# Optimization experiments

Measured on AMD Instinct MI355X. Metric: run time of the kernel, lower is better.

## Reference

```python
import jax, jax.numpy as jnp
import numpy as np

M = 128      # max_child_num
H = 256      # hidden_size
F = 256      # node_feat_size (must equal H per original view logic)
T = 4        # edge_type_num
I = 2        # num_iterations
NSEM = 57    # Tree.num_sem


def setup_inputs() -> dict:
    key = jax.random.key(0)
    ks = jax.random.split(key, 16)
    def lin(k, shape, fan_in):
        return (jax.random.normal(k, shape, jnp.float32) / np.sqrt(fan_in)).astype(jnp.float32)
    return {
        "parent_feature": jax.random.normal(ks[0], (1, F), jnp.float32),
        "W_parent": lin(ks[1], (F, H * M), F),
        "b_parent": jnp.zeros((H * M,), jnp.float32),
        "W_exists": lin(ks[2], (H, 1), H),
        "b_exists": jnp.zeros((1,), jnp.float32),
        "W_edge_latent": lin(ks[3], (2 * H, H), 2 * H),
        "b_edge_latent": jnp.zeros((H,), jnp.float32),
        "W_edge_exists": lin(ks[4], (T, H), H),   # per-type 1-out linear, stacked
        "b_edge_exists": jnp.zeros((T,), jnp.float32),
        "W_op": lin(ks[5], (I, 3 * H + T, H), 3 * H + T),
        "b_op": jnp.zeros((I, H), jnp.float32),
        "W_child": lin(ks[6], (H * (I + 1), H), H * (I + 1)),
        "b_child": jnp.zeros((H,), jnp.float32),
        "W_sem": lin(ks[7], (H, NSEM), H),
        "b_sem": jnp.zeros((NSEM,), jnp.float32),
        "W_child2": lin(ks[8], (H, F), H),
        "b_child2": jnp.zeros((F,), jnp.float32),
    }


def reference(parent_feature, W_parent, b_parent, W_exists, b_exists,
              W_edge_latent, b_edge_latent, W_edge_exists, b_edge_exists,
              W_op, b_op, W_child, b_child, W_sem, b_sem, W_child2, b_child2):
    # parent -> per-child latents [M, H]
    cf = jax.nn.relu(parent_feature @ W_parent + b_parent).reshape(M, H)
    child_exists_logits = cf @ W_exists + b_exists                      # [M, 1]

    # pairwise edge latents [M, M, H]
    pair = jnp.concatenate([
        jnp.broadcast_to(cf[:, None, :], (M, M, H)),
        jnp.broadcast_to(cf[None, :, :], (M, M, H)),
    ], axis=-1)
    el = jax.nn.relu(pair @ W_edge_latent + b_edge_latent)              # [M, M, H]
    ee = jnp.einsum('ijh,th->ijt', el, W_edge_exists) + b_edge_exists   # [M, M, T]

    # dense-mask equivalent of torch.nonzero edge list: an edge exists per
    # (i, j, type) triple where its logit > 0 and both endpoints exist.
    exists = child_exists_logits[:, 0] > 0                              # [M]
    mask = (ee > 0) & exists[:, None, None] & exists[None, :, None]     # [M, M, T]
    maskf = mask.astype(cf.dtype)

    iter_feats = [cf]
    for i in range(I):
        # node_edge_op input is concat([cf_src, cf_dst, edge_latent, onehot(t)*logit]);
        # split the linear into per-block matmuls to avoid a [M,M,T,3H+T] concat.
        W1, W2, W3, W4 = (W_op[i, :H], W_op[i, H:2 * H],
                          W_op[i, 2 * H:3 * H], W_op[i, 3 * H:])        # W4: [T, H]
        pre = ((cf @ W1)[:, None, None, :]
               + (cf @ W2)[None, :, None, :]
               + (el @ W3)[:, :, None, :]
               + ee[:, :, :, None] * W4[None, None, :, :]
               + b_op[i])                                               # [M, M, T, H]
        h = jax.nn.relu(pre) * maskf[..., None]
        # scatter_max over source index i with zero-initialized output:
        # relu output >= 0 and masked-out edges are 0, so plain max matches.
        cf = jnp.max(h, axis=(1, 2))                                    # [M, H]
        iter_feats.append(cf)

    allf = jnp.concatenate(iter_feats, axis=1)                          # [M, H*(I+1)]
    ch = jax.nn.relu(allf @ W_child + b_child)                          # [M, H]
    child_sem_logits = ch @ W_sem + b_sem                               # [M, NSEM]
    child_feats = jax.nn.relu(ch @ W_child2 + b_child2)                 # [M, F]

    return (child_feats[None], child_sem_logits[None],
            child_exists_logits[None], ee[None])
```

## Files before the change

### kernel.cpp

```cpp
#include <hip/hip_runtime.h>
#include <hip/hip_bf16.h>

#define M_ 128
#define H_ 256
#define F_ 256
#define T_ 4
#define NSEM_ 57

typedef __attribute__((ext_vector_type(8))) short bf16x8;
typedef __attribute__((ext_vector_type(4))) float f32x4;

__device__ __forceinline__ float4 ld4(const float* p) { return *reinterpret_cast<const float4*>(p); }
__device__ __forceinline__ void st4(float* p, float4 v) { *reinterpret_cast<float4*>(p) = v; }
__device__ __forceinline__ float4 add4(float4 a, float4 b) { return make_float4(a.x+b.x, a.y+b.y, a.z+b.z, a.w+b.w); }
__device__ __forceinline__ float4 relu4(float4 a) { return make_float4(fmaxf(a.x,0.f), fmaxf(a.y,0.f), fmaxf(a.z,0.f), fmaxf(a.w,0.f)); }
__device__ __forceinline__ float4 fma4(float s, float4 w, float4 c) { return make_float4(fmaf(s,w.x,c.x), fmaf(s,w.y,c.y), fmaf(s,w.z,c.z), fmaf(s,w.w,c.w)); }

__device__ __forceinline__ unsigned short f2bfu(float x) {
  unsigned u = __float_as_uint(x);
  return (unsigned short)((u + 0x7FFFu + ((u >> 16) & 1u)) >> 16);
}
__device__ __forceinline__ unsigned pack2(float lo, float hi) {
  return (unsigned)f2bfu(lo) | ((unsigned)f2bfu(hi) << 16);
}

__global__ void __launch_bounds__(256) k_parent(
    const float* __restrict__ pf, const float* __restrict__ Wp,
    const float* __restrict__ Wop, float* __restrict__ part,
    unsigned short* __restrict__ W36F, unsigned short* __restrict__ W768F)
{
  const int t = threadIdx.x;
  __shared__ float spf[8];
  __shared__ float tile[16][17];

  const int fbg = blockIdx.x >> 1;
  const int half = blockIdx.x & 1;
  const bool it0 = fbg < 128;
  const int fb = it0 ? fbg : fbg - 128;
  const int kk = fb >> 4, ct = fb & 15;
  const int base_k = kk * 32 + half * 16;
  int row_base;
  if (it0) row_base = 512 + base_k;
  else row_base = (base_k < 256) ? 512 + base_k
                : (base_k < 512 ? base_k : base_k - 512);
  const float* wsrc = Wop + (it0 ? 0 : 197632);
  {
    const int r = t >> 4, c = t & 15;
    tile[r][c] = wsrc[(size_t)(row_base + r) * 256 + ct * 16 + c];
  }

  const int cb = (blockIdx.x & 31) * 1024 + t * 4;
  const int kc = blockIdx.x >> 5;
  if (t < 8) spf[t] = pf[kc * 8 + t];
  __syncthreads();
  const float* w = Wp + (size_t)kc * 8 * 32768 + cb;
  float4 acc = make_float4(0.f, 0.f, 0.f, 0.f);
  #pragma unroll
  for (int k = 0; k < 8; ++k)
    acc = fma4(spf[k], ld4(w + (size_t)k * 32768), acc);
  st4(&part[kc * 32768 + cb], acc);

  {
    const int k_local = ((t >> 7) << 3) + (t & 7);
    const int h_local = (t >> 3) & 15;
    const int e = half * 256 + t;
    unsigned short v = f2bfu(tile[k_local][h_local]);
    if (it0) W36F[fb * 512 + e] = v;
    else     W768F[fb * 512 + e] = v;
  }
}

__global__ void __launch_bounds__(256) k_stage1(
    const float* __restrict__ part, const float* __restrict__ bp,
    const float* __restrict__ Wel, const float* __restrict__ Wop0,
    const float* __restrict__ Wex, const float* __restrict__ bex,
    float* __restrict__ cf0, float* __restrict__ A, float* __restrict__ B,
    float* __restrict__ a1, float* __restrict__ a2,
    float* __restrict__ cf1, float* __restrict__ cf2,
    float* __restrict__ out_ex)
{
  const int m = blockIdx.x >> 1, sel = blockIdx.x & 1;
  const int t = threadIdx.x;
  __shared__ float sall[256];
  __shared__ float red[2][4][256];
  __shared__ float redE[4];

  (sel ? cf2 : cf1)[m * 256 + t] = 0.f;

  float pv[32];
  #pragma unroll
  for (int q = 0; q < 32; ++q) pv[q] = part[q * 32768 + m * 256 + t];
  float v = bp[m * 256 + t];
  #pragma unroll
  for (int q = 0; q < 32; ++q) v += pv[q];
  v = fmaxf(v, 0.f);
  sall[t] = v;
  if (sel == 0) {
    cf0[m * 256 + t] = v;
    float p = v * Wex[t];
    #pragma unroll
    for (int off = 32; off > 0; off >>= 1) p += __shfl_xor(p, off);
    if ((t & 63) == 0) redE[t >> 6] = p;
  }
  __syncthreads();

  const float* W0 = Wel  + (sel ? 65536 : 0);
  const float* W1 = Wop0 + (sel ? 65536 : 0);
  const int hq = (t & 63) << 2, kg = t >> 6, k0 = kg * 64;
  float4 acc0 = make_float4(0.f, 0.f, 0.f, 0.f), acc1 = acc0;
  #pragma unroll 8
  for (int k = k0; k < k0 + 64; ++k) {
    const float s = sall[k];
    acc0 = fma4(s, ld4(W0 + k * 256 + hq), acc0);
    acc1 = fma4(s, ld4(W1 + k * 256 + hq), acc1);
  }
  st4(&red[0][kg][hq], acc0);
  st4(&red[1][kg][hq], acc1);
  __syncthreads();
  if (kg < 2) {
    float4 r = add4(add4(ld4(&red[kg][0][hq]), ld4(&red[kg][1][hq])),
                    add4(ld4(&red[kg][2][hq]), ld4(&red[kg][3][hq])));
    float* dst = (kg == 0) ? (sel ? B : A) : (sel ? a2 : a1);
    st4(&dst[m * 256 + hq], r);
  }
  if (sel == 0 && t == 0)
    out_ex[m] = redE[0] + redE[1] + redE[2] + redE[3] + bex[0];
}

__global__ void __launch_bounds__(512) k_gemm0(
    const float* __restrict__ Arow, const float* __restrict__ Brow,
    const float* __restrict__ bel, const unsigned short* __restrict__ W36F,
    const float* __restrict__ Wee, const float* __restrict__ bee,
    const float* __restrict__ a1, const float* __restrict__ a2,
    const float* __restrict__ Wop0, const float* __restrict__ bop0,
    const float* __restrict__ exlog,
    float* __restrict__ ee_g, float* __restrict__ cf1)
{
  const int i  = blockIdx.x >> 2;
  const int jq = blockIdx.x & 3;
  const int t  = threadIdx.x;
  const int w  = t >> 6;
  const int l  = t & 63;
  __shared__ char sEL[32 * 512];
  __shared__ float see[32][4];
  __shared__ float sexf[32];

  const bool exi = exlog[i] > 0.f;
  const int lr = l & 15, lk = l >> 4;

  const int c0 = w * 32 + lr, c1 = c0 + 16;
  const float b10 = a1[i * 256 + c0] + bop0[c0];
  const float b11 = a1[i * 256 + c1] + bop0[c1];
  float w40[4], w41[4], a2v0[8], a2v1[8];
  #pragma unroll
  for (int tt = 0; tt < 4; ++tt) {
    w40[tt] = Wop0[(768 + tt) * 256 + c0];
    w41[tt] = Wop0[(768 + tt) * 256 + c1];
  }
  #pragma unroll
  for (int jt = 0; jt < 2; ++jt)
    #pragma unroll
    for (int q = 0; q < 4; ++q) {
      const int j = jq * 32 + jt * 16 + lk * 4 + q;
      a2v0[jt * 4 + q] = a2[j * 256 + c0];
      a2v1[jt * 4 + q] = a2[j * 256 + c1];
    }

  {
    const int row = t >> 4;
    const int sub = t & 15;
    const int kb  = sub * 16;
    const float* Ap  = Arow + i * 256 + kb;
    const float* Bp  = Brow + (jq * 32 + row) * 256 + kb;
    const float* blp = bel + kb;
    float e[16];
    #pragma unroll
    for (int q = 0; q < 16; q += 4) {
      float4 av = ld4(Ap + q), bv = ld4(Bp + q), lv = ld4(blp + q);
      e[q+0] = fmaxf(av.x + bv.x + lv.x, 0.f);
      e[q+1] = fmaxf(av.y + bv.y + lv.y, 0.f);
      e[q+2] = fmaxf(av.z + bv.z + lv.z, 0.f);
      e[q+3] = fmaxf(av.w + bv.w + lv.w, 0.f);
    }
    float s[4] = {0.f, 0.f, 0.f, 0.f};
    #pragma unroll
    for (int tt = 0; tt < 4; ++tt) {
      #pragma unroll
      for (int q = 0; q < 16; q += 4) {
        float4 wv = ld4(Wee + tt * 256 + kb + q);
        s[tt] = fmaf(e[q+0], wv.x, s[tt]);
        s[tt] = fmaf(e[q+1], wv.y, s[tt]);
        s[tt] = fmaf(e[q+2], wv.z, s[tt]);
        s[tt] = fmaf(e[q+3], wv.w, s[tt]);
      }
    }
    #pragma unroll
    for (int off = 1; off < 16; off <<= 1) {
      s[0] += __shfl_xor(s[0], off);
      s[1] += __shfl_xor(s[1], off);
      s[2] += __shfl_xor(s[2], off);
      s[3] += __shfl_xor(s[3], off);
    }
    if (sub < 4) {
      const float v = s[sub] + bee[sub];
      see[row][sub] = v;
      ee_g[(i * 128 + jq * 32 + row) * 4 + sub] = v;
    }
    const int swz = (row & 7) << 4;
    uint4 w0, w1;
    w0.x = pack2(e[0], e[1]);  w0.y = pack2(e[2], e[3]);
    w0.z = pack2(e[4], e[5]);  w0.w = pack2(e[6], e[7]);
    w1.x = pack2(e[8], e[9]);  w1.y = pack2(e[10], e[11]);
    w1.z = pack2(e[12], e[13]); w1.w = pack2(e[14], e[15]);
    *reinterpret_cast<uint4*>(sEL + ((row * 512 + kb * 2)      ^ swz)) = w0;
    *reinterpret_cast<uint4*>(sEL + ((row * 512 + kb * 2 + 16) ^ swz)) = w1;
  }
  if (t < 32) sexf[t] = exlog[jq * 32 + t];
  __syncthreads();

  f32x4 acc[2][2];
  #pragma unroll
  for (int jt = 0; jt < 2; ++jt)
    #pragma unroll
    for (int ct = 0; ct < 2; ++ct)
      acc[jt][ct] = (f32x4){0.f, 0.f, 0.f, 0.f};

  const int swz0 = (lr & 7) << 4;
  bf16x8 cb0 = *reinterpret_cast<const bf16x8*>(W36F + (0 * 16 + w * 2 + 0) * 512 + l * 8);
  bf16x8 cb1 = *reinterpret_cast<const bf16x8*>(W36F + (0 * 16 + w * 2 + 1) * 512 + l * 8);
  bf16x8 ca0 = *reinterpret_cast<const bf16x8*>(sEL + ((lr * 512 + lk * 16) ^ swz0));
  bf16x8 ca1 = *reinterpret_cast<const bf16x8*>(sEL + (((16 + lr) * 512 + lk * 16) ^ swz0));
  #pragma unroll
  for (int kc = 0; kc < 8; ++kc) {
    bf16x8 nb0, nb1, na0, na1;
    if (kc < 7) {
      const int kbyte = (kc + 1) * 64 + lk * 16;
      nb0 = *reinterpret_cast<const bf16x8*>(W36F + ((kc + 1) * 16 + w * 2 + 0) * 512 + l * 8);
      nb1 = *reinterpret_cast<const bf16x8*>(W36F + ((kc + 1) * 16 + w * 2 + 1) * 512 + l * 8);
      na0 = *reinterpret_cast<const bf16x8*>(sEL + ((lr * 512 + kbyte) ^ swz0));
      na1 = *reinterpret_cast<const bf16x8*>(sEL + (((16 + lr) * 512 + kbyte) ^ swz0));
    }
    acc[0][0] = __builtin_amdgcn_mfma_f32_16x16x32_bf16(ca0, cb0, acc[0][0], 0, 0, 0);
    acc[1][0] = __builtin_amdgcn_mfma_f32_16x16x32_bf16(ca1, cb0, acc[1][0], 0, 0, 0);
    acc[0][1] = __builtin_amdgcn_mfma_f32_16x16x32_bf16(ca0, cb1, acc[0][1], 0, 0, 0);
    acc[1][1] = __builtin_amdgcn_mfma_f32_16x16x32_bf16(ca1, cb1, acc[1][1], 0, 0, 0);
    if (kc < 7) { cb0 = nb0; cb1 = nb1; ca0 = na0; ca1 = na1; }
  }

  float am0 = 0.f, am1 = 0.f;
  #pragma unroll
  for (int jt = 0; jt < 2; ++jt) {
    #pragma unroll
    for (int q = 0; q < 4; ++q) {
      const int jrow = jt * 16 + lk * 4 + q;
      if (exi && (sexf[jrow] > 0.f)) {
        const float e0 = see[jrow][0], e1 = see[jrow][1];
        const float e2 = see[jrow][2], e3 = see[jrow][3];
        const float pb0 = b10 + a2v0[jt * 4 + q] + acc[jt][0][q];
        const float pb1 = b11 + a2v1[jt * 4 + q] + acc[jt][1][q];
        if (e0 > 0.f) { am0 = fmaxf(am0, fmaxf(fmaf(e0, w40[0], pb0), 0.f));
                        am1 = fmaxf(am1, fmaxf(fmaf(e0, w41[0], pb1), 0.f)); }
        if (e1 > 0.f) { am0 = fmaxf(am0, fmaxf(fmaf(e1, w40[1], pb0), 0.f));
                        am1 = fmaxf(am1, fmaxf(fmaf(e1, w41[1], pb1), 0.f)); }
        if (e2 > 0.f) { am0 = fmaxf(am0, fmaxf(fmaf(e2, w40[2], pb0), 0.f));
                        am1 = fmaxf(am1, fmaxf(fmaf(e2, w41[2], pb1), 0.f)); }
        if (e3 > 0.f) { am0 = fmaxf(am0, fmaxf(fmaf(e3, w40[3], pb0), 0.f));
                        am1 = fmaxf(am1, fmaxf(fmaf(e3, w41[3], pb1), 0.f)); }
      }
    }
  }
  am0 = fmaxf(am0, __shfl_xor(am0, 16));
  am0 = fmaxf(am0, __shfl_xor(am0, 32));
  am1 = fmaxf(am1, __shfl_xor(am1, 16));
  am1 = fmaxf(am1, __shfl_xor(am1, 32));
  if (lk == 0) {
    atomicMax((unsigned int*)&cf1[i * 256 + c0], __float_as_uint(am0));
    atomicMax((unsigned int*)&cf1[i * 256 + c1], __float_as_uint(am1));
  }
}

__global__ void __launch_bounds__(512) k_gemm1(
    const float* __restrict__ Arow, const float* __restrict__ Brow,
    const float* __restrict__ bel, const unsigned short* __restrict__ W768F,
    const float* __restrict__ cf1,
    const float* __restrict__ Wop1, const float* __restrict__ bop1,
    const float* __restrict__ exlog, const float* __restrict__ ee_g,
    float* __restrict__ cf2)
{
  const int i  = blockIdx.x >> 2;
  const int jq = blockIdx.x & 3;
  const int t  = threadIdx.x;
  const int w  = t >> 6;
  const int l  = t & 63;
  __shared__ char sEL[32 * 1536];
  __shared__ float see[32][4];
  __shared__ float sexf[32];

  const bool exi = exlog[i] > 0.f;
  const int lr = l & 15, lk = l >> 4;

  const int c0 = w * 32 + lr, c1 = c0 + 16;
  const float b10 = bop1[c0];
  const float b11 = bop1[c1];
  float w40[4], w41[4];
  #pragma unroll
  for (int tt = 0; tt < 4; ++tt) {
    w40[tt] = Wop1[(768 + tt) * 256 + c0];
    w41[tt] = Wop1[(768 + tt) * 256 + c1];
  }
  if (t < 128)
    see[t >> 2][t & 3] = ee_g[(i * 128 + jq * 32 + (t >> 2)) * 4 + (t & 3)];
  if (t < 32) sexf[t] = exlog[jq * 32 + t];

  {
    const int row = t >> 4;
    const int sub = t & 15;
    const int kb  = sub * 16;
    const int swz = (row & 7) << 4;
    {
      const float* Ap  = Arow + i * 256 + kb;
      const float* Bp  = Brow + (jq * 32 + row) * 256 + kb;
      const float* blp = bel + kb;
      float e[16];
      #pragma unroll
      for (int q = 0; q < 16; q += 4) {
        float4 av = ld4(Ap + q), bv = ld4(Bp + q), lv = ld4(blp + q);
        e[q+0] = fmaxf(av.x + bv.x + lv.x, 0.f);
        e[q+1] = fmaxf(av.y + bv.y + lv.y, 0.f);
        e[q+2] = fmaxf(av.z + bv.z + lv.z, 0.f);
        e[q+3] = fmaxf(av.w + bv.w + lv.w, 0.f);
      }
      uint4 w0, w1;
      w0.x = pack2(e[0], e[1]);  w0.y = pack2(e[2], e[3]);
      w0.z = pack2(e[4], e[5]);  w0.w = pack2(e[6], e[7]);
      w1.x = pack2(e[8], e[9]);  w1.y = pack2(e[10], e[11]);
      w1.z = pack2(e[12], e[13]); w1.w = pack2(e[14], e[15]);
      *reinterpret_cast<uint4*>(sEL + ((row * 1536 + kb * 2)      ^ swz)) = w0;
      *reinterpret_cast<uint4*>(sEL + ((row * 1536 + kb * 2 + 16) ^ swz)) = w1;
    }
    {
      const float* cj = cf1 + (jq * 32 + row) * 256 + kb;
      float4 v0 = ld4(cj), v1 = ld4(cj + 4), v2 = ld4(cj + 8), v3 = ld4(cj + 12);
      uint4 w0, w1;
      w0.x = pack2(v0.x, v0.y); w0.y = pack2(v0.z, v0.w);
      w0.z = pack2(v1.x, v1.y); w0.w = pack2(v1.z, v1.w);
      w1.x = pack2(v2.x, v2.y); w1.y = pack2(v2.z, v2.w);
      w1.z = pack2(v3.x, v3.y); w1.w = pack2(v3.z, v3.w);
      *reinterpret_cast<uint4*>(sEL + ((row * 1536 + 512 + kb * 2)      ^ swz)) = w0;
      *reinterpret_cast<uint4*>(sEL + ((row * 1536 + 512 + kb * 2 + 16) ^ swz)) = w1;
    }
    {
      const float* ci = cf1 + i * 256 + kb;
      float4 v0 = ld4(ci), v1 = ld4(ci + 4), v2 = ld4(ci + 8), v3 = ld4(ci + 12);
      uint4 w0, w1;
      w0.x = pack2(v0.x, v0.y); w0.y = pack2(v0.z, v0.w);
      w0.z = pack2(v1.x, v1.y); w0.w = pack2(v1.z, v1.w);
      w1.x = pack2(v2.x, v2.y); w1.y = pack2(v2.z, v2.w);
      w1.z = pack2(v3.x, v3.y); w1.w = pack2(v3.z, v3.w);
      *reinterpret_cast<uint4*>(sEL + ((row * 1536 + 1024 + kb * 2)      ^ swz)) = w0;
      *reinterpret_cast<uint4*>(sEL + ((row * 1536 + 1024 + kb * 2 + 16) ^ swz)) = w1;
    }
  }
  __syncthreads();

  f32x4 acc[2][2];
  #pragma unroll
  for (int jt = 0; jt < 2; ++jt)
    #pragma unroll
    for (int ct = 0; ct < 2; ++ct)
      acc[jt][ct] = (f32x4){0.f, 0.f, 0.f, 0.f};

  const int swz0 = (lr & 7) << 4;
  bf16x8 cb0 = *reinterpret_cast<const bf16x8*>(W768F + (0 * 16 + w * 2 + 0) * 512 + l * 8);
  bf16x8 cb1 = *reinterpret_cast<const bf16x8*>(W768F + (0 * 16 + w * 2 + 1) * 512 + l * 8);
  bf16x8 ca0 = *reinterpret_cast<const bf16x8*>(sEL + ((lr * 1536 + lk * 16) ^ swz0));
  bf16x8 ca1 = *reinterpret_cast<const bf16x8*>(sEL + (((16 + lr) * 1536 + lk * 16) ^ swz0));
  #pragma unroll
  for (int kc = 0; kc < 24; ++kc) {
    bf16x8 nb0, nb1, na0, na1;
    if (kc < 23) {
      const int kbyte = (kc + 1) * 64 + lk * 16;
      nb0 = *reinterpret_cast<const bf16x8*>(W768F + ((kc + 1) * 16 + w * 2 + 0) * 512 + l * 8);
      nb1 = *reinterpret_cast<const bf16x8*>(W768F + ((kc + 1) * 16 + w * 2 + 1) * 512 + l * 8);
      na0 = *reinterpret_cast<const bf16x8*>(sEL + ((lr * 1536 + kbyte) ^ swz0));
      na1 = *reinterpret_cast<const bf16x8*>(sEL + (((16 + lr) * 1536 + kbyte) ^ swz0));
    }
    acc[0][0] = __builtin_amdgcn_mfma_f32_16x16x32_bf16(ca0, cb0, acc[0][0], 0, 0, 0);
    acc[1][0] = __builtin_amdgcn_mfma_f32_16x16x32_bf16(ca1, cb0, acc[1][0], 0, 0, 0);
    acc[0][1] = __builtin_amdgcn_mfma_f32_16x16x32_bf16(ca0, cb1, acc[0][1], 0, 0, 0);
    acc[1][1] = __builtin_amdgcn_mfma_f32_16x16x32_bf16(ca1, cb1, acc[1][1], 0, 0, 0);
    if (kc < 23) { cb0 = nb0; cb1 = nb1; ca0 = na0; ca1 = na1; }
  }

  float am0 = 0.f, am1 = 0.f;
  #pragma unroll
  for (int jt = 0; jt < 2; ++jt) {
    #pragma unroll
    for (int q = 0; q < 4; ++q) {
      const int jrow = jt * 16 + lk * 4 + q;
      if (exi && (sexf[jrow] > 0.f)) {
        const float e0 = see[jrow][0], e1 = see[jrow][1];
        const float e2 = see[jrow][2], e3 = see[jrow][3];
        const float pb0 = b10 + acc[jt][0][q];
        const float pb1 = b11 + acc[jt][1][q];
        if (e0 > 0.f) { am0 = fmaxf(am0, fmaxf(fmaf(e0, w40[0], pb0), 0.f));
                        am1 = fmaxf(am1, fmaxf(fmaf(e0, w41[0], pb1), 0.f)); }
        if (e1 > 0.f) { am0 = fmaxf(am0, fmaxf(fmaf(e1, w40[1], pb0), 0.f));
                        am1 = fmaxf(am1, fmaxf(fmaf(e1, w41[1], pb1), 0.f)); }
        if (e2 > 0.f) { am0 = fmaxf(am0, fmaxf(fmaf(e2, w40[2], pb0), 0.f));
                        am1 = fmaxf(am1, fmaxf(fmaf(e2, w41[2], pb1), 0.f)); }
        if (e3 > 0.f) { am0 = fmaxf(am0, fmaxf(fmaf(e3, w40[3], pb0), 0.f));
                        am1 = fmaxf(am1, fmaxf(fmaf(e3, w41[3], pb1), 0.f)); }
      }
    }
  }
  am0 = fmaxf(am0, __shfl_xor(am0, 16));
  am0 = fmaxf(am0, __shfl_xor(am0, 32));
  am1 = fmaxf(am1, __shfl_xor(am1, 16));
  am1 = fmaxf(am1, __shfl_xor(am1, 32));
  if (lk == 0) {
    atomicMax((unsigned int*)&cf2[i * 256 + c0], __float_as_uint(am0));
    atomicMax((unsigned int*)&cf2[i * 256 + c1], __float_as_uint(am1));
  }
}

__global__ void __launch_bounds__(512) k_final(
    const float* __restrict__ cf0, const float* __restrict__ cf1,
    const float* __restrict__ cf2,
    const float* __restrict__ Wch, const float* __restrict__ bch,
    const float* __restrict__ Wsem, const float* __restrict__ bsem,
    const float* __restrict__ Wch2, const float* __restrict__ bch2,
    float* __restrict__ out_feats, float* __restrict__ out_sem)
{
  const int m  = blockIdx.x;
  const int t  = threadIdx.x;
  const int hq = (t & 63) << 2;
  const int kg = t >> 6;
  __shared__ float sall[768];
  __shared__ float sch[256];
  __shared__ float red[8][256];
  __shared__ float redS[8][64];

  if (t < 256) {
    sall[t]       = cf0[m * 256 + t];
    sall[256 + t] = cf1[m * 256 + t];
    sall[512 + t] = cf2[m * 256 + t];
  }
  __syncthreads();

  {
    float4 acc = make_float4(0.f, 0.f, 0.f, 0.f);
    const int k0 = kg * 96;
    #pragma unroll 8
    for (int k = k0; k < k0 + 96; ++k)
      acc = fma4(sall[k], ld4(Wch + k * 256 + hq), acc);
    st4(&red[kg][hq], acc);
  }
  __syncthreads();
  if (kg == 0) {
    float4 r = ld4(&red[0][hq]);
    #pragma unroll
    for (int g2 = 1; g2 < 8; ++g2) r = add4(r, ld4(&red[g2][hq]));
    r = relu4(add4(r, ld4(bch + hq)));
    st4(&sch[hq], r);
  }
  __syncthreads();

  {
    float4 f = make_float4(0.f, 0.f, 0.f, 0.f);
    const int k0 = kg * 32;
    #pragma unroll 8
    for (int k = k0; k < k0 + 32; ++k)
      f = fma4(sch[k], ld4(Wch2 + k * 256 + hq), f);
    const int s = t & 63;
    float sv = 0.f;
    if (s < 57) {
      #pragma unroll 8
      for (int k = k0; k < k0 + 32; ++k)
        sv = fmaf(sch[k], Wsem[k * 57 + s], sv);
    }
    redS[kg][s] = sv;
    st4(&red[kg][hq], f);
  }
  __syncthreads();
  if (kg == 0) {
    float4 r = ld4(&red[0][hq]);
    #pragma unroll
    for (int g2 = 1; g2 < 8; ++g2) r = add4(r, ld4(&red[g2][hq]));
    r = relu4(add4(r, ld4(bch2 + hq)));
    st4(&out_feats[m * 256 + hq], r);
  }
  if (t < 57) {
    float s2 = bsem[t];
    #pragma unroll
    for (int g2 = 0; g2 < 8; ++g2) s2 += redS[g2][t];
    out_sem[m * 57 + t] = s2;
  }
}

extern "C" void kernel_launch(void* const* d_in, const int* in_sizes, int n_in,
                              void* d_out, int out_size, void* d_ws, size_t ws_size,
                              hipStream_t stream)
{
  const float* pf   = (const float*)d_in[0];
  const float* Wp   = (const float*)d_in[1];
  const float* bp   = (const float*)d_in[2];
  const float* Wex  = (const float*)d_in[3];
  const float* bex  = (const float*)d_in[4];
  const float* Wel  = (const float*)d_in[5];
  const float* bel  = (const float*)d_in[6];
  const float* Wee  = (const float*)d_in[7];
  const float* bee  = (const float*)d_in[8];
  const float* Wop  = (const float*)d_in[9];
  const float* bop  = (const float*)d_in[10];
  const float* Wch  = (const float*)d_in[11];
  const float* bch  = (const float*)d_in[12];
  const float* Wsem = (const float*)d_in[13];
  const float* bsem = (const float*)d_in[14];
  const float* Wch2 = (const float*)d_in[15];
  const float* bch2 = (const float*)d_in[16];

  float* out_feats = (float*)d_out;
  float* out_sem   = out_feats + M_ * F_;
  float* out_ex    = out_sem + M_ * NSEM_;
  float* out_ee    = out_ex + M_;

  float* ws = (float*)d_ws;
  float* cf0 = ws;
  float* cf1 = ws + 32768;
  float* cf2 = ws + 65536;
  float* Ab  = ws + 98304;
  float* Bb  = ws + 131072;
  float* a1  = ws + 163840;
  float* a2  = ws + 196608;
  float* part = ws + 229376;
  unsigned short* W36F  = (unsigned short*)(ws + 1277952);
  unsigned short* W768F = (unsigned short*)(ws + 1310720);

  const float* Wop0 = Wop;
  const float* Wop1 = Wop + 197632;

  k_parent<<<1024, 256, 0, stream>>>(pf, Wp, Wop, part, W36F, W768F);
  k_stage1<<<256, 256, 0, stream>>>(part, bp, Wel, Wop0, Wex, bex,
                                    cf0, Ab, Bb, a1, a2, cf1, cf2, out_ex);
  k_gemm0<<<512, 512, 0, stream>>>(Ab, Bb, bel, W36F, Wee, bee,
                                   a1, a2, Wop0, bop, out_ex, out_ee, cf1);
  k_gemm1<<<512, 512, 0, stream>>>(Ab, Bb, bel, W768F, cf1,
                                   Wop1, bop + 256, out_ex, out_ee, cf2);
  k_final<<<128, 512, 0, stream>>>(cf0, cf1, cf2, Wch, bch, Wsem, bsem,
                                   Wch2, bch2, out_feats, out_sem);
}
```

Baseline: 65.41 us.

## Enlarge edge GEMM tiles to 64 rows and merge stage1 blocks per child

The two pairwise edge GEMM kernels now give each block 64 j-rows instead of 32, so each weight fragment loaded from global memory feeds four MFMA row tiles rather than two. This halves the grid and halves how often the B operand is reloaded across blocks. The explicit register double-buffering of operands is dropped in favour of straight loads inside the unrolled loop. Stage1 now runs one 512-thread block per child, so the parent reduction is done once instead of twice. The trade-offs are fewer blocks (256) on a large GPU, more LDS per block (96KB in gemm1), and a2 now read from global memory inside the epilogue.

```diff
diff --git a/kernel.cpp b/kernel.cpp
--- a/kernel.cpp
+++ b/kernel.cpp
@@ -70,7 +70,7 @@
   }
 }
 
-__global__ void __launch_bounds__(256) k_stage1(
+__global__ void __launch_bounds__(512) k_stage1(
     const float* __restrict__ part, const float* __restrict__ bp,
     const float* __restrict__ Wel, const float* __restrict__ Wop0,
     const float* __restrict__ Wex, const float* __restrict__ bex,
@@ -79,51 +79,48 @@
     float* __restrict__ cf1, float* __restrict__ cf2,
     float* __restrict__ out_ex)
 {
-  const int m = blockIdx.x >> 1, sel = blockIdx.x & 1;
+  const int m = blockIdx.x;
   const int t = threadIdx.x;
+  const int tt = t & 255, half = t >> 8;
   __shared__ float sall[256];
-  __shared__ float red[2][4][256];
+  __shared__ float red[8][256];
   __shared__ float redE[4];
 
-  (sel ? cf2 : cf1)[m * 256 + t] = 0.f;
-
-  float pv[32];
-  #pragma unroll
-  for (int q = 0; q < 32; ++q) pv[q] = part[q * 32768 + m * 256 + t];
-  float v = bp[m * 256 + t];
-  #pragma unroll
-  for (int q = 0; q < 32; ++q) v += pv[q];
-  v = fmaxf(v, 0.f);
-  sall[t] = v;
-  if (sel == 0) {
-    cf0[m * 256 + t] = v;
-    float p = v * Wex[t];
+  (half ? cf2 : cf1)[m * 256 + tt] = 0.f;
+
+  if (half == 0) {
+    float pv[32];
+    #pragma unroll
+    for (int q = 0; q < 32; ++q) pv[q] = part[q * 32768 + m * 256 + tt];
+    float v = bp[m * 256 + tt];
+    #pragma unroll
+    for (int q = 0; q < 32; ++q) v += pv[q];
+    v = fmaxf(v, 0.f);
+    sall[tt] = v;
+    cf0[m * 256 + tt] = v;
+    float p = v * Wex[tt];
     #pragma unroll
     for (int off = 32; off > 0; off >>= 1) p += __shfl_xor(p, off);
-    if ((t & 63) == 0) redE[t >> 6] = p;
-  }
-  __syncthreads();
-
-  const float* W0 = Wel  + (sel ? 65536 : 0);
-  const float* W1 = Wop0 + (sel ? 65536 : 0);
-  const int hq = (t & 63) << 2, kg = t >> 6, k0 = kg * 64;
-  float4 acc0 = make_float4(0.f, 0.f, 0.f, 0.f), acc1 = acc0;
+    if ((tt & 63) == 0) redE[tt >> 6] = p;
+  }
+  __syncthreads();
+
+  const int kg = t >> 6, s = kg & 3, kh = kg >> 2;
+  const int hq = (t & 63) << 2, k0 = kh * 128;
+  const float* W = (s == 0) ? Wel : (s == 1) ? Wel + 65536
+                 : (s == 2) ? Wop0 : Wop0 + 65536;
+  float4 acc = make_float4(0.f, 0.f, 0.f, 0.f);
   #pragma unroll 8
-  for (int k = k0; k < k0 + 64; ++k) {
-    const float s = sall[k];
-    acc0 = fma4(s, ld4(W0 + k * 256 + hq), acc0);
-    acc1 = fma4(s, ld4(W1 + k * 256 + hq), acc1);
-  }
-  st4(&red[0][kg][hq], acc0);
-  st4(&red[1][kg][hq], acc1);
-  __syncthreads();
-  if (kg < 2) {
-    float4 r = add4(add4(ld4(&red[kg][0][hq]), ld4(&red[kg][1][hq])),
-                    add4(ld4(&red[kg][2][hq]), ld4(&red[kg][3][hq])));
-    float* dst = (kg == 0) ? (sel ? B : A) : (sel ? a2 : a1);
+  for (int k = k0; k < k0 + 128; ++k)
+    acc = fma4(sall[k], ld4(W + k * 256 + hq), acc);
+  st4(&red[kg][hq], acc);
+  __syncthreads();
+  if (kg < 4) {
+    float4 r = add4(ld4(&red[kg][hq]), ld4(&red[kg + 4][hq]));
+    float* dst = (kg == 0) ? A : (kg == 1) ? B : (kg == 2) ? a1 : a2;
     st4(&dst[m * 256 + hq], r);
   }
-  if (sel == 0 && t == 0)
+  if (t == 0)
     out_ex[m] = redE[0] + redE[1] + redE[2] + redE[3] + bex[0];
 }
 
@@ -136,46 +133,37 @@
     const float* __restrict__ exlog,
     float* __restrict__ ee_g, float* __restrict__ cf1)
 {
-  const int i  = blockIdx.x >> 2;
-  const int jq = blockIdx.x & 3;
+  const int i  = blockIdx.x >> 1;
+  const int jh = blockIdx.x & 1;
   const int t  = threadIdx.x;
   const int w  = t >> 6;
   const int l  = t & 63;
-  __shared__ char sEL[32 * 512];
-  __shared__ float see[32][4];
-  __shared__ float sexf[32];
+  __shared__ char sEL[64 * 512];
+  __shared__ float see[64][4];
+  __shared__ float sexf[64];
 
   const bool exi = exlog[i] > 0.f;
   const int lr = l & 15, lk = l >> 4;
-
   const int c0 = w * 32 + lr, c1 = c0 + 16;
   const float b10 = a1[i * 256 + c0] + bop0[c0];
   const float b11 = a1[i * 256 + c1] + bop0[c1];
-  float w40[4], w41[4], a2v0[8], a2v1[8];
-  #pragma unroll
-  for (int tt = 0; tt < 4; ++tt) {
-    w40[tt] = Wop0[(768 + tt) * 256 + c0];
-    w41[tt] = Wop0[(768 + tt) * 256 + c1];
-  }
-  #pragma unroll
-  for (int jt = 0; jt < 2; ++jt)
-    #pragma unroll
-    for (int q = 0; q < 4; ++q) {
-      const int j = jq * 32 + jt * 16 + lk * 4 + q;
-      a2v0[jt * 4 + q] = a2[j * 256 + c0];
-      a2v1[jt * 4 + q] = a2[j * 256 + c1];
-    }
+  float w40[4], w41[4];
+  #pragma unroll
+  for (int q = 0; q < 4; ++q) {
+    w40[q] = Wop0[(768 + q) * 256 + c0];
+    w41[q] = Wop0[(768 + q) * 256 + c1];
+  }
 
   {
-    const int row = t >> 4;
-    const int sub = t & 15;
-    const int kb  = sub * 16;
+    const int row = t >> 3;
+    const int sub = t & 7;
+    const int kb  = sub * 32;
     const float* Ap  = Arow + i * 256 + kb;
-    const float* Bp  = Brow + (jq * 32 + row) * 256 + kb;
+    const float* Bp  = Brow + (jh * 64 + row) * 256 + kb;
     const float* blp = bel + kb;
-    float e[16];
-    #pragma unroll
-    for (int q = 0; q < 16; q += 4) {
+    float e[32];
+    #pragma unroll
+    for (int q = 0; q < 32; q += 4) {
       float4 av = ld4(Ap + q), bv = ld4(Bp + q), lv = ld4(blp + q);
       e[q+0] = fmaxf(av.x + bv.x + lv.x, 0.f);
       e[q+1] = fmaxf(av.y + bv.y + lv.y, 0.f);
@@ -186,7 +174,7 @@
     #pragma unroll
     for (int tt = 0; tt < 4; ++tt) {
       #pragma unroll
-      for (int q = 0; q < 16; q += 4) {
+      for (int q = 0; q < 32; q += 4) {
         float4 wv = ld4(Wee + tt * 256 + kb + q);
         s[tt] = fmaf(e[q+0], wv.x, s[tt]);
         s[tt] = fmaf(e[q+1], wv.y, s[tt]);
@@ -195,7 +183,7 @@
       }
     }
     #pragma unroll
-    for (int off = 1; off < 16; off <<= 1) {
+    for (int off = 1; off < 8; off <<= 1) {
       s[0] += __shfl_xor(s[0], off);
       s[1] += __shfl_xor(s[1], off);
       s[2] += __shfl_xor(s[2], off);
@@ -204,60 +192,56 @@
     if (sub < 4) {
       const float v = s[sub] + bee[sub];
       see[row][sub] = v;
-      ee_g[(i * 128 + jq * 32 + row) * 4 + sub] = v;
+      ee_g[(i * 128 + jh * 64 + row) * 4 + sub] = v;
     }
     const int swz = (row & 7) << 4;
-    uint4 w0, w1;
-    w0.x = pack2(e[0], e[1]);  w0.y = pack2(e[2], e[3]);
-    w0.z = pack2(e[4], e[5]);  w0.w = pack2(e[6], e[7]);
-    w1.x = pack2(e[8], e[9]);  w1.y = pack2(e[10], e[11]);
-    w1.z = pack2(e[12], e[13]); w1.w = pack2(e[14], e[15]);
-    *reinterpret_cast<uint4*>(sEL + ((row * 512 + kb * 2)      ^ swz)) = w0;
-    *reinterpret_cast<uint4*>(sEL + ((row * 512 + kb * 2 + 16) ^ swz)) = w1;
-  }
-  if (t < 32) sexf[t] = exlog[jq * 32 + t];
-  __syncthreads();
-
-  f32x4 acc[2][2];
-  #pragma unroll
-  for (int jt = 0; jt < 2; ++jt)
+    #pragma unroll
+    for (int h4 = 0; h4 < 4; ++h4) {
+      uint4 wv;
+      wv.x = pack2(e[h4*8+0], e[h4*8+1]);
+      wv.y = pack2(e[h4*8+2], e[h4*8+3]);
+      wv.z = pack2(e[h4*8+4], e[h4*8+5]);
+      wv.w = pack2(e[h4*8+6], e[h4*8+7]);
+      *reinterpret_cast<uint4*>(sEL + ((row * 512 + kb * 2 + h4 * 16) ^ swz)) = wv;
+    }
+  }
+  if (t < 64) sexf[t] = exlog[jh * 64 + t];
+  __syncthreads();
+
+  f32x4 acc[4][2];
+  #pragma unroll
+  for (int rt = 0; rt < 4; ++rt)
     #pragma unroll
     for (int ct = 0; ct < 2; ++ct)
-      acc[jt][ct] = (f32x4){0.f, 0.f, 0.f, 0.f};
+      acc[rt][ct] = (f32x4){0.f, 0.f, 0.f, 0.f};
 
   const int swz0 = (lr & 7) << 4;
-  bf16x8 cb0 = *reinterpret_cast<const bf16x8*>(W36F + (0 * 16 + w * 2 + 0) * 512 + l * 8);
-  bf16x8 cb1 = *reinterpret_cast<const bf16x8*>(W36F + (0 * 16 + w * 2 + 1) * 512 + l * 8);
-  bf16x8 ca0 = *reinterpret_cast<const bf16x8*>(sEL + ((lr * 512 + lk * 16) ^ swz0));
-  bf16x8 ca1 = *reinterpret_cast<const bf16x8*>(sEL + (((16 + lr) * 512 + lk * 16) ^ swz0));
   #pragma unroll
   for (int kc = 0; kc < 8; ++kc) {
-    bf16x8 nb0, nb1, na0, na1;
-    if (kc < 7) {
-      const int kbyte = (kc + 1) * 64 + lk * 16;
-      nb0 = *reinterpret_cast<const bf16x8*>(W36F + ((kc + 1) * 16 + w * 2 + 0) * 512 + l * 8);
-      nb1 = *reinterpret_cast<const bf16x8*>(W36F + ((kc + 1) * 16 + w * 2 + 1) * 512 + l * 8);
-      na0 = *reinterpret_cast<const bf16x8*>(sEL + ((lr * 512 + kbyte) ^ swz0));
-      na1 = *reinterpret_cast<const bf16x8*>(sEL + (((16 + lr) * 512 + kbyte) ^ swz0));
-    }
-    acc[0][0] = __builtin_amdgcn_mfma_f32_16x16x32_bf16(ca0, cb0, acc[0][0], 0, 0, 0);
-    acc[1][0] = __builtin_amdgcn_mfma_f32_16x16x32_bf16(ca1, cb0, acc[1][0], 0, 0, 0);
-    acc[0][1] = __builtin_amdgcn_mfma_f32_16x16x32_bf16(ca0, cb1, acc[0][1], 0, 0, 0);
-    acc[1][1] = __builtin_amdgcn_mfma_f32_16x16x32_bf16(ca1, cb1, acc[1][1], 0, 0, 0);
-    if (kc < 7) { cb0 = nb0; cb1 = nb1; ca0 = na0; ca1 = na1; }
+    const int kbyte = kc * 64 + lk * 16;
+    bf16x8 bf0 = *reinterpret_cast<const bf16x8*>(W36F + (kc * 16 + w * 2 + 0) * 512 + l * 8);
+    bf16x8 bf1 = *reinterpret_cast<const bf16x8*>(W36F + (kc * 16 + w * 2 + 1) * 512 + l * 8);
+    #pragma unroll
+    for (int rt = 0; rt < 4; ++rt) {
+      bf16x8 af = *reinterpret_cast<const bf16x8*>(
+          sEL + (((rt * 16 + lr) * 512 + kbyte) ^ swz0));
+      acc[rt][0] = __builtin_amdgcn_mfma_f32_16x16x32_bf16(af, bf0, acc[rt][0], 0, 0, 0);
+      acc[rt][1] = __builtin_amdgcn_mfma_f32_16x16x32_bf16(af, bf1, acc[rt][1], 0, 0, 0);
+    }
   }
 
   float am0 = 0.f, am1 = 0.f;
   #pragma unroll
-  for (int jt = 0; jt < 2; ++jt) {
+  for (int rt = 0; rt < 4; ++rt) {
     #pragma unroll
     for (int q = 0; q < 4; ++q) {
-      const int jrow = jt * 16 + lk * 4 + q;
+      const int jrow = rt * 16 + lk * 4 + q;
+      const int j = jh * 64 + jrow;
       if (exi && (sexf[jrow] > 0.f)) {
         const float e0 = see[jrow][0], e1 = see[jrow][1];
         const float e2 = see[jrow][2], e3 = see[jrow][3];
-        const float pb0 = b10 + a2v0[jt * 4 + q] + acc[jt][0][q];
-        const float pb1 = b11 + a2v1[jt * 4 + q] + acc[jt][1][q];
+        const float pb0 = b10 + a2[j * 256 + c0] + acc[rt][0][q];
+        const float pb1 = b11 + a2[j * 256 + c1] + acc[rt][1][q];
         if (e0 > 0.f) { am0 = fmaxf(am0, fmaxf(fmaf(e0, w40[0], pb0), 0.f));
                         am1 = fmaxf(am1, fmaxf(fmaf(e0, w41[0], pb1), 0.f)); }
         if (e1 > 0.f) { am0 = fmaxf(am0, fmaxf(fmaf(e1, w40[1], pb0), 0.f));
@@ -287,122 +271,116 @@
     const float* __restrict__ exlog, const float* __restrict__ ee_g,
     float* __restrict__ cf2)
 {
-  const int i  = blockIdx.x >> 2;
-  const int jq = blockIdx.x & 3;
+  const int i  = blockIdx.x >> 1;
+  const int jh = blockIdx.x & 1;
   const int t  = threadIdx.x;
   const int w  = t >> 6;
   const int l  = t & 63;
-  __shared__ char sEL[32 * 1536];
-  __shared__ float see[32][4];
-  __shared__ float sexf[32];
+  __shared__ char sEL[64 * 1536];
+  __shared__ float see[64][4];
+  __shared__ float sexf[64];
 
   const bool exi = exlog[i] > 0.f;
   const int lr = l & 15, lk = l >> 4;
-
   const int c0 = w * 32 + lr, c1 = c0 + 16;
   const float b10 = bop1[c0];
   const float b11 = bop1[c1];
   float w40[4], w41[4];
   #pragma unroll
-  for (int tt = 0; tt < 4; ++tt) {
-    w40[tt] = Wop1[(768 + tt) * 256 + c0];
-    w41[tt] = Wop1[(768 + tt) * 256 + c1];
-  }
-  if (t < 128)
-    see[t >> 2][t & 3] = ee_g[(i * 128 + jq * 32 + (t >> 2)) * 4 + (t & 3)];
-  if (t < 32) sexf[t] = exlog[jq * 32 + t];
+  for (int q = 0; q < 4; ++q) {
+    w40[q] = Wop1[(768 + q) * 256 + c0];
+    w41[q] = Wop1[(768 + q) * 256 + c1];
+  }
+  if (t < 256)
+    see[t >> 2][t & 3] = ee_g[(i * 128 + jh * 64 + (t >> 2)) * 4 + (t & 3)];
+  if (t < 64) sexf[t] = exlog[jh * 64 + t];
 
   {
-    const int row = t >> 4;
-    const int sub = t & 15;
-    const int kb  = sub * 16;
+    const int row = t >> 3;
+    const int sub = t & 7;
+    const int kb  = sub * 32;
     const int swz = (row & 7) << 4;
     {
       const float* Ap  = Arow + i * 256 + kb;
-      const float* Bp  = Brow + (jq * 32 + row) * 256 + kb;
+      const float* Bp  = Brow + (jh * 64 + row) * 256 + kb;
       const float* blp = bel + kb;
-      float e[16];
+      float e[32];
       #pragma unroll
-      for (int q = 0; q < 16; q += 4) {
+      for (int q = 0; q < 32; q += 4) {
         float4 av = ld4(Ap + q), bv = ld4(Bp + q), lv = ld4(blp + q);
         e[q+0] = fmaxf(av.x + bv.x + lv.x, 0.f);
         e[q+1] = fmaxf(av.y + bv.y + lv.y, 0.f);
         e[q+2] = fmaxf(av.z + bv.z + lv.z, 0.f);
         e[q+3] = fmaxf(av.w + bv.w + lv.w, 0.f);
       }
-      uint4 w0, w1;
-      w0.x = pack2(e[0], e[1]);  w0.y = pack2(e[2], e[3]);
-      w0.z = pack2(e[4], e[5]);  w0.w = pack2(e[6], e[7]);
-      w1.x = pack2(e[8], e[9]);  w1.y = pack2(e[10], e[11]);
-      w1.z = pack2(e[12], e[13]); w1.w = pack2(e[14], e[15]);
-      *reinterpret_cast<uint4*>(sEL + ((row * 1536 + kb * 2)      ^ swz)) = w0;
-      *reinterpret_cast<uint4*>(sEL + ((row * 1536 + kb * 2 + 16) ^ swz)) = w1;
+      #pragma unroll
+      for (int h4 = 0; h4 < 4; ++h4) {
+        uint4 wv;
+        wv.x = pack2(e[h4*8+0], e[h4*8+1]);
+        wv.y = pack2(e[h4*8+2], e[h4*8+3]);
+        wv.z = pack2(e[h4*8+4], e[h4*8+5]);
+        wv.w = pack2(e[h4*8+6], e[h4*8+7]);
+        *reinterpret_cast<uint4*>(sEL + ((row * 1536 + kb * 2 + h4 * 16) ^ swz)) = wv;
+      }
     }
     {
-      const float* cj = cf1 + (jq * 32 + row) * 256 + kb;
-      float4 v0 = ld4(cj), v1 = ld4(cj + 4), v2 = ld4(cj + 8), v3 = ld4(cj + 12);
-      uint4 w0, w1;
-      w0.x = pack2(v0.x, v0.y); w0.y = pack2(v0.z, v0.w);
-      w0.z = pack2(v1.x, v1.y); w0.w = pack2(v1.z, v1.w);
-      w1.x = pack2(v2.x, v2.y); w1.y = pack2(v2.z, v2.w);
-      w1.z = pack2(v3.x, v3.y); w1.w = pack2(v3.z, v3.w);
-      *reinterpret_cast<uint4*>(sEL + ((row * 1536 + 512 + kb * 2)      ^ swz)) = w0;
-      *reinterpret_cast<uint4*>(sEL + ((row * 1536 + 512 + kb * 2 + 16) ^ swz)) = w1;
+      const float* cj = cf1 + (jh * 64 + row) * 256 + kb;
+      #pragma unroll
+      for (int h4 = 0; h4 < 4; ++h4) {
+        float4 v0 = ld4(cj + h4 * 8), v1 = ld4(cj + h4 * 8 + 4);
+        uint4 wv;
+        wv.x = pack2(v0.x, v0.y); wv.y = pack2(v0.z, v0.w);
+        wv.z = pack2(v1.x, v1.y); wv.w = pack2(v1.z, v1.w);
+        *reinterpret_cast<uint4*>(sEL + ((row * 1536 + 512 + kb * 2 + h4 * 16) ^ swz)) = wv;
+      }
     }
     {
       const float* ci = cf1 + i * 256 + kb;
-      float4 v0 = ld4(ci), v1 = ld4(ci + 4), v2 = ld4(ci + 8), v3 = ld4(ci + 12);
-      uint4 w0, w1;
-      w0.x = pack2(v0.x, v0.y); w0.y = pack2(v0.z, v0.w);
-      w0.z = pack2(v1.x, v1.y); w0.w = pack2(v1.z, v1.w);
-      w1.x = pack2(v2.x, v2.y); w1.y = pack2(v2.z, v2.w);
-      w1.z = pack2(v3.x, v3.y); w1.w = pack2(v3.z, v3.w);
-      *reinterpret_cast<uint4*>(sEL + ((row * 1536 + 1024 + kb * 2)      ^ swz)) = w0;
-      *reinterpret_cast<uint4*>(sEL + ((row * 1536 + 1024 + kb * 2 + 16) ^ swz)) = w1;
-    }
-  }
-  __syncthreads();
-
-  f32x4 acc[2][2];
-  #pragma unroll
-  for (int jt = 0; jt < 2; ++jt)
+      #pragma unroll
+      for (int h4 = 0; h4 < 4; ++h4) {
+        float4 v0 = ld4(ci + h4 * 8), v1 = ld4(ci + h4 * 8 + 4);
+        uint4 wv;
+        wv.x = pack2(v0.x, v0.y); wv.y = pack2(v0.z, v0.w);
+        wv.z = pack2(v1.x, v1.y); wv.w = pack2(v1.z, v1.w);
+        *reinterpret_cast<uint4*>(sEL + ((row * 1536 + 1024 + kb * 2 + h4 * 16) ^ swz)) = wv;
+      }
+    }
+  }
+  __syncthreads();
+
+  f32x4 acc[4][2];
+  #pragma unroll
+  for (int rt = 0; rt < 4; ++rt)
     #pragma unroll
     for (int ct = 0; ct < 2; ++ct)
-      acc[jt][ct] = (f32x4){0.f, 0.f, 0.f, 0.f};
+      acc[rt][ct] = (f32x4){0.f, 0.f, 0.f, 0.f};
 
   const int swz0 = (lr & 7) << 4;
-  bf16x8 cb0 = *reinterpret_cast<const bf16x8*>(W768F + (0 * 16 + w * 2 + 0) * 512 + l * 8);
-  bf16x8 cb1 = *reinterpret_cast<const bf16x8*>(W768F + (0 * 16 + w * 2 + 1) * 512 + l * 8);
-  bf16x8 ca0 = *reinterpret_cast<const bf16x8*>(sEL + ((lr * 1536 + lk * 16) ^ swz0));
-  bf16x8 ca1 = *reinterpret_cast<const bf16x8*>(sEL + (((16 + lr) * 1536 + lk * 16) ^ swz0));
   #pragma unroll
   for (int kc = 0; kc < 24; ++kc) {
-    bf16x8 nb0, nb1, na0, na1;
-    if (kc < 23) {
-      const int kbyte = (kc + 1) * 64 + lk * 16;
-      nb0 = *reinterpret_cast<const bf16x8*>(W768F + ((kc + 1) * 16 + w * 2 + 0) * 512 + l * 8);
-      nb1 = *reinterpret_cast<const bf16x8*>(W768F + ((kc + 1) * 16 + w * 2 + 1) * 512 + l * 8);
-      na0 = *reinterpret_cast<const bf16x8*>(sEL + ((lr * 1536 + kbyte) ^ swz0));
-      na1 = *reinterpret_cast<const bf16x8*>(sEL + (((16 + lr) * 1536 + kbyte) ^ swz0));
-    }
-    acc[0][0] = __builtin_amdgcn_mfma_f32_16x16x32_bf16(ca0, cb0, acc[0][0], 0, 0, 0);
-    acc[1][0] = __builtin_amdgcn_mfma_f32_16x16x32_bf16(ca1, cb0, acc[1][0], 0, 0, 0);
-    acc[0][1] = __builtin_amdgcn_mfma_f32_16x16x32_bf16(ca0, cb1, acc[0][1], 0, 0, 0);
-    acc[1][1] = __builtin_amdgcn_mfma_f32_16x16x32_bf16(ca1, cb1, acc[1][1], 0, 0, 0);
-    if (kc < 23) { cb0 = nb0; cb1 = nb1; ca0 = na0; ca1 = na1; }
+    const int kbyte = kc * 64 + lk * 16;
+    bf16x8 bf0 = *reinterpret_cast<const bf16x8*>(W768F + (kc * 16 + w * 2 + 0) * 512 + l * 8);
+    bf16x8 bf1 = *reinterpret_cast<const bf16x8*>(W768F + (kc * 16 + w * 2 + 1) * 512 + l * 8);
+    #pragma unroll
+    for (int rt = 0; rt < 4; ++rt) {
+      bf16x8 af = *reinterpret_cast<const bf16x8*>(
+          sEL + (((rt * 16 + lr) * 1536 + kbyte) ^ swz0));
+      acc[rt][0] = __builtin_amdgcn_mfma_f32_16x16x32_bf16(af, bf0, acc[rt][0], 0, 0, 0);
+      acc[rt][1] = __builtin_amdgcn_mfma_f32_16x16x32_bf16(af, bf1, acc[rt][1], 0, 0, 0);
+    }
   }
 
   float am0 = 0.f, am1 = 0.f;
   #pragma unroll
-  for (int jt = 0; jt < 2; ++jt) {
+  for (int rt = 0; rt < 4; ++rt) {
     #pragma unroll
     for (int q = 0; q < 4; ++q) {
-      const int jrow = jt * 16 + lk * 4 + q;
+      const int jrow = rt * 16 + lk * 4 + q;
       if (exi && (sexf[jrow] > 0.f)) {
         const float e0 = see[jrow][0], e1 = see[jrow][1];
         const float e2 = see[jrow][2], e3 = see[jrow][3];
-        const float pb0 = b10 + acc[jt][0][q];
-        const float pb1 = b11 + acc[jt][1][q];
+        const float pb0 = b10 + acc[rt][0][q];
+        const float pb1 = b11 + acc[rt][1][q];
         if (e0 > 0.f) { am0 = fmaxf(am0, fmaxf(fmaf(e0, w40[0], pb0), 0.f));
                         am1 = fmaxf(am1, fmaxf(fmaf(e0, w41[0], pb1), 0.f)); }
         if (e1 > 0.f) { am0 = fmaxf(am0, fmaxf(fmaf(e1, w40[1], pb0), 0.f));
@@ -541,11 +519,11 @@
   const float* Wop1 = Wop + 197632;
 
   k_parent<<<1024, 256, 0, stream>>>(pf, Wp, Wop, part, W36F, W768F);
-  k_stage1<<<256, 256, 0, stream>>>(part, bp, Wel, Wop0, Wex, bex,
+  k_stage1<<<128, 512, 0, stream>>>(part, bp, Wel, Wop0, Wex, bex,
                                     cf0, Ab, Bb, a1, a2, cf1, cf2, out_ex);
-  k_gemm0<<<512, 512, 0, stream>>>(Ab, Bb, bel, W36F, Wee, bee,
+  k_gemm0<<<256, 512, 0, stream>>>(Ab, Bb, bel, W36F, Wee, bee,
                                    a1, a2, Wop0, bop, out_ex, out_ee, cf1);
-  k_gemm1<<<512, 512, 0, stream>>>(Ab, Bb, bel, W768F, cf1,
+  k_gemm1<<<256, 512, 0, stream>>>(Ab, Bb, bel, W768F, cf1,
                                    Wop1, bop + 256, out_ex, out_ee, cf2);
   k_final<<<128, 512, 0, stream>>>(cf0, cf1, cf2, Wch, bch, Wsem, bsem,
                                    Wch2, bch2, out_feats, out_sem);
```

After: 82.42 us. 1.26x slower.
